# Optimization experiments

Hardware: AMD Instinct MI355X
Metric: run time of the kernel (lower is better)

The kernel has to match this reference:

```python
import jax, jax.numpy as jnp
import numpy as np

B, T, C = 4, 2048, 1024
N_HEAD = 16
HEAD_DIM = C // N_HEAD
SCALE = 1.0 / np.sqrt(HEAD_DIM).astype(np.float32)


def setup_inputs() -> dict:
    key = jax.random.key(0)
    k1, k2, k3 = jax.random.split(key, 3)
    x = jax.random.normal(k1, (B, T, C), dtype=jnp.float32)
    # torch Linear weights: [out_features, in_features], scaled init
    w_qkv = jax.random.normal(k2, (3 * C, C), dtype=jnp.float32) * (1.0 / np.sqrt(C))
    w_out = jax.random.normal(k3, (C, C), dtype=jnp.float32) * (1.0 / np.sqrt(C))
    b_out = jnp.zeros((C,), dtype=jnp.float32)
    return {"x": x, "w_qkv": w_qkv, "w_out": w_out, "b_out": b_out}


def reference(x, w_qkv, w_out, b_out):
    Bsz, Tlen, Cdim = x.shape
    qkv = jnp.einsum('btc,oc->bto', x, w_qkv)  # [B,T,3C]
    q, k, v = jnp.split(qkv, 3, axis=-1)
    # [B,H,T,D]
    def heads(t):
        return t.reshape(Bsz, Tlen, N_HEAD, HEAD_DIM).transpose(0, 2, 1, 3)
    q, k, v = heads(q), heads(k), heads(v)
    att = jnp.einsum('bhqd,bhkd->bhqk', q, k) * SCALE  # [B,H,T,T]
    causal = jnp.tril(jnp.ones((Tlen, Tlen), dtype=bool))
    att = jnp.where(causal[None, None], att, -jnp.inf)
    att = jax.nn.softmax(att, axis=-1)
    out = jnp.einsum('bhqk,bhkd->bhqd', att, v)
    out = out.transpose(0, 2, 1, 3).reshape(Bsz, Tlen, Cdim)
    out = jnp.einsum('btc,oc->bto', out, w_out) + b_out
    return out
```

## Files before the change

kernel.cpp:

```cpp
#include <hip/hip_runtime.h>
#include <stdint.h>


typedef __attribute__((ext_vector_type(8))) short bf16x8;
typedef __attribute__((ext_vector_type(4))) float f32x4;

#define EXP2F(x) __builtin_amdgcn_exp2f(x)
#define SL2E 0.18033688011112042f
#define FIXED_M 15.0f

template <bool B> struct BoolC { static constexpr bool value = B; };

__device__ __forceinline__ short f2bf(float f) {
  union { float f; unsigned u; } c; c.f = f;
  unsigned u = c.u;
  unsigned r = (u + 0x7fffu + ((u >> 16) & 1u)) >> 16;
  return (short)(unsigned short)r;
}

__device__ __forceinline__ void softmax_pack(const f32x4* sc, bf16x8& pa0, bf16x8& pa1) {
  union U { int i[4]; bf16x8 v; };
  U u0, u1;
#pragma unroll
  for (int j = 0; j < 4; ++j) {
    float p0 = EXP2F(sc[j][0]);
    float p1 = EXP2F(sc[j][1]);
    float p2 = EXP2F(sc[j][2]);
    float p3 = EXP2F(sc[j][3]);
    int w0, w1;
    asm("v_cvt_pk_bf16_f32 %0, %1, %2" : "=v"(w0) : "v"(p0), "v"(p1));
    asm("v_cvt_pk_bf16_f32 %0, %1, %2" : "=v"(w1) : "v"(p2), "v"(p3));
    if (j < 2) { u0.i[j * 2] = w0; u0.i[j * 2 + 1] = w1; }
    else       { u1.i[(j - 2) * 2] = w0; u1.i[(j - 2) * 2 + 1] = w1; }
  }
  pa0 = u0.v;
  pa1 = u1.v;
}

__device__ __forceinline__ void llds16(const short* g, short* l) {
  __builtin_amdgcn_global_load_lds(
      (const __attribute__((address_space(1))) unsigned int*)g,
      (__attribute__((address_space(3))) unsigned int*)l, 16, 0, 0);
}

__global__ __launch_bounds__(256) void cast_all(
    const float* __restrict__ x, const float* __restrict__ wq,
    const float* __restrict__ wo, short* __restrict__ xb,
    short* __restrict__ wqb, short* __restrict__ wob) {
  const int b = blockIdx.x;
  const float* src;
  short* dst;
  int idx;
  if (b < 8192)        { src = x;  dst = xb;  idx = b * 256 + threadIdx.x; }
  else if (b < 11264)  { src = wq; dst = wqb; idx = (b - 8192) * 256 + threadIdx.x; }
  else                 { src = wo; dst = wob; idx = (b - 11264) * 256 + threadIdx.x; }
  float4 f = ((const float4*)src)[idx];
  short4 o;
  o.x = f2bf(f.x); o.y = f2bf(f.y); o.z = f2bf(f.z); o.w = f2bf(f.w);
  ((short4*)dst)[idx] = o;
}

__global__ __launch_bounds__(512) void gemm_qkv(
    const short* __restrict__ A, const short* __restrict__ Bw,
    short* __restrict__ Qo, short* __restrict__ Ko, short* __restrict__ Vt) {
  const int K = 1024;
  __shared__ short smem[49152];
  const int tid = threadIdx.x;
  const int lane = tid & 63;
  const int wave = tid >> 6;
  const int wr = wave >> 1;
  const int wc = wave & 1;
  const int m0 = blockIdx.y * 256;
  const int n0 = blockIdx.x * 128;
  const int mrow = lane & 15;
  const int kq = lane >> 4;

  f32x4 acc[4][4];
#pragma unroll
  for (int i = 0; i < 4; ++i)
#pragma unroll
    for (int j = 0; j < 4; ++j) acc[i][j] = (f32x4){0.f, 0.f, 0.f, 0.f};

  auto stageA = [&](int t, int buf, int ca) {
    const int c = ca * 512 + tid;
    const int row = c >> 3;
    const int sc = (c & 7) ^ (row & 7);
    llds16(A + (size_t)(m0 + row) * K + t * 64 + sc * 8,
           &smem[buf * 24576 + c * 8]);
  };
  auto stageB = [&](int t, int buf, int cb) {
    const int c = cb * 512 + tid;
    const int row = c >> 3;
    const int sc = (c & 7) ^ (row & 7);
    llds16(Bw + (size_t)(n0 + row) * K + t * 64 + sc * 8,
           &smem[buf * 24576 + 16384 + c * 8]);
  };

  auto rdA = [&](const short* lA, int i, int kk) -> bf16x8 {
    const int row = wr * 64 + i * 16 + mrow;
    const int ch = (kq + 4 * kk) ^ (row & 7);
    return *(const bf16x8*)&lA[row * 64 + ch * 8];
  };
  auto rdB = [&](const short* lB, int j, int kk) -> bf16x8 {
    const int row = wc * 64 + j * 16 + mrow;
    const int ch = (kq + 4 * kk) ^ (row & 7);
    return *(const bf16x8*)&lB[row * 64 + ch * 8];
  };

  stageA(0, 0, 0); stageA(0, 0, 1); stageA(0, 0, 2); stageA(0, 0, 3);
  stageB(0, 0, 0); stageB(0, 0, 1);
  asm volatile("s_waitcnt vmcnt(0)" ::: "memory");
  __syncthreads();

#define PHASE_TAIL()                                         \
  __builtin_amdgcn_s_barrier();                              \
  asm volatile("s_waitcnt lgkmcnt(0)" ::: "memory");         \
  __builtin_amdgcn_sched_barrier(0);                         \
  __builtin_amdgcn_s_setprio(1);

#define PHASE_END()                                          \
  __builtin_amdgcn_s_setprio(0);                             \
  __builtin_amdgcn_sched_barrier(0);                         \
  __builtin_amdgcn_s_barrier();

  for (int t = 0; t < 16; ++t) {
    const int buf = t & 1;
    const int nb = buf ^ 1;
    const short* lA = &smem[buf * 24576];
    const short* lB = lA + 16384;
    bf16x8 a0, a1, a2, a3, bf0, bf1, bf2, bf3;

    a0 = rdA(lA, 0, 0); a1 = rdA(lA, 1, 0);
    bf0 = rdB(lB, 0, 0); bf1 = rdB(lB, 1, 0);
    bf2 = rdB(lB, 2, 0); bf3 = rdB(lB, 3, 0);
    if (t < 15) { stageA(t + 1, nb, 0); stageA(t + 1, nb, 1); }
    PHASE_TAIL();
    acc[0][0] = __builtin_amdgcn_mfma_f32_16x16x32_bf16(a0, bf0, acc[0][0], 0, 0, 0);
    acc[0][1] = __builtin_amdgcn_mfma_f32_16x16x32_bf16(a0, bf1, acc[0][1], 0, 0, 0);
    acc[0][2] = __builtin_amdgcn_mfma_f32_16x16x32_bf16(a0, bf2, acc[0][2], 0, 0, 0);
    acc[0][3] = __builtin_amdgcn_mfma_f32_16x16x32_bf16(a0, bf3, acc[0][3], 0, 0, 0);
    acc[1][0] = __builtin_amdgcn_mfma_f32_16x16x32_bf16(a1, bf0, acc[1][0], 0, 0, 0);
    acc[1][1] = __builtin_amdgcn_mfma_f32_16x16x32_bf16(a1, bf1, acc[1][1], 0, 0, 0);
    acc[1][2] = __builtin_amdgcn_mfma_f32_16x16x32_bf16(a1, bf2, acc[1][2], 0, 0, 0);
    acc[1][3] = __builtin_amdgcn_mfma_f32_16x16x32_bf16(a1, bf3, acc[1][3], 0, 0, 0);
    PHASE_END();

    a2 = rdA(lA, 2, 0); a3 = rdA(lA, 3, 0);
    if (t < 15) { stageA(t + 1, nb, 2); stageA(t + 1, nb, 3); }
    PHASE_TAIL();
    acc[2][0] = __builtin_amdgcn_mfma_f32_16x16x32_bf16(a2, bf0, acc[2][0], 0, 0, 0);
    acc[2][1] = __builtin_amdgcn_mfma_f32_16x16x32_bf16(a2, bf1, acc[2][1], 0, 0, 0);
    acc[2][2] = __builtin_amdgcn_mfma_f32_16x16x32_bf16(a2, bf2, acc[2][2], 0, 0, 0);
    acc[2][3] = __builtin_amdgcn_mfma_f32_16x16x32_bf16(a2, bf3, acc[2][3], 0, 0, 0);
    acc[3][0] = __builtin_amdgcn_mfma_f32_16x16x32_bf16(a3, bf0, acc[3][0], 0, 0, 0);
    acc[3][1] = __builtin_amdgcn_mfma_f32_16x16x32_bf16(a3, bf1, acc[3][1], 0, 0, 0);
    acc[3][2] = __builtin_amdgcn_mfma_f32_16x16x32_bf16(a3, bf2, acc[3][2], 0, 0, 0);
    acc[3][3] = __builtin_amdgcn_mfma_f32_16x16x32_bf16(a3, bf3, acc[3][3], 0, 0, 0);
    PHASE_END();

    a0 = rdA(lA, 0, 1); a1 = rdA(lA, 1, 1);
    bf0 = rdB(lB, 0, 1); bf1 = rdB(lB, 1, 1);
    bf2 = rdB(lB, 2, 1); bf3 = rdB(lB, 3, 1);
    if (t < 15) { stageB(t + 1, nb, 0); stageB(t + 1, nb, 1); }
    PHASE_TAIL();
    acc[0][0] = __builtin_amdgcn_mfma_f32_16x16x32_bf16(a0, bf0, acc[0][0], 0, 0, 0);
    acc[0][1] = __builtin_amdgcn_mfma_f32_16x16x32_bf16(a0, bf1, acc[0][1], 0, 0, 0);
    acc[0][2] = __builtin_amdgcn_mfma_f32_16x16x32_bf16(a0, bf2, acc[0][2], 0, 0, 0);
    acc[0][3] = __builtin_amdgcn_mfma_f32_16x16x32_bf16(a0, bf3, acc[0][3], 0, 0, 0);
    acc[1][0] = __builtin_amdgcn_mfma_f32_16x16x32_bf16(a1, bf0, acc[1][0], 0, 0, 0);
    acc[1][1] = __builtin_amdgcn_mfma_f32_16x16x32_bf16(a1, bf1, acc[1][1], 0, 0, 0);
    acc[1][2] = __builtin_amdgcn_mfma_f32_16x16x32_bf16(a1, bf2, acc[1][2], 0, 0, 0);
    acc[1][3] = __builtin_amdgcn_mfma_f32_16x16x32_bf16(a1, bf3, acc[1][3], 0, 0, 0);
    PHASE_END();

    a2 = rdA(lA, 2, 1); a3 = rdA(lA, 3, 1);
    PHASE_TAIL();
    acc[2][0] = __builtin_amdgcn_mfma_f32_16x16x32_bf16(a2, bf0, acc[2][0], 0, 0, 0);
    acc[2][1] = __builtin_amdgcn_mfma_f32_16x16x32_bf16(a2, bf1, acc[2][1], 0, 0, 0);
    acc[2][2] = __builtin_amdgcn_mfma_f32_16x16x32_bf16(a2, bf2, acc[2][2], 0, 0, 0);
    acc[2][3] = __builtin_amdgcn_mfma_f32_16x16x32_bf16(a2, bf3, acc[2][3], 0, 0, 0);
    acc[3][0] = __builtin_amdgcn_mfma_f32_16x16x32_bf16(a3, bf0, acc[3][0], 0, 0, 0);
    acc[3][1] = __builtin_amdgcn_mfma_f32_16x16x32_bf16(a3, bf1, acc[3][1], 0, 0, 0);
    acc[3][2] = __builtin_amdgcn_mfma_f32_16x16x32_bf16(a3, bf2, acc[3][2], 0, 0, 0);
    acc[3][3] = __builtin_amdgcn_mfma_f32_16x16x32_bf16(a3, bf3, acc[3][3], 0, 0, 0);
    __builtin_amdgcn_s_setprio(0);
    __builtin_amdgcn_sched_barrier(0);
    if (t < 15) asm volatile("s_waitcnt vmcnt(0)" ::: "memory");
    __builtin_amdgcn_s_barrier();
  }
#undef PHASE_TAIL
#undef PHASE_END

  __syncthreads();

  const int b = m0 >> 11;
  if (n0 < 2048) {
    const float sc_ = ((n0 >> 10) == 1) ? SL2E : 1.0f;
    short* lC = smem;
#pragma unroll
    for (int i = 0; i < 4; ++i) {
      const int rl = wr * 64 + i * 16 + kq * 4;
#pragma unroll
      for (int j = 0; j < 4; ++j) {
        const int col = wc * 64 + j * 16 + mrow;
#pragma unroll
        for (int r = 0; r < 4; ++r)
          lC[(rl + r) * 132 + col] = f2bf(acc[i][j][r] * sc_);
      }
    }
    __syncthreads();
    short* dst = (n0 >> 10) == 0 ? Qo : Ko;
#pragma unroll
    for (int call = 0; call < 8; ++call) {
      const int cc = call * 512 + tid;
      const int row = cc >> 4;
      const int ch = cc & 15;
      const int t = (m0 & 2047) + row;
      const int c = (n0 + ch * 8) & 1023;
      const int h = c >> 6;
      const int d = c & 63;
      bf16x8 val = *(const bf16x8*)&lC[row * 132 + ch * 8];
      *(bf16x8*)(dst + ((size_t)(b * 16 + h) * 2048 + t) * 64 + d) = val;
    }
  } else {
    short* lCt = smem;
#pragma unroll
    for (int i = 0; i < 4; ++i) {
      const int rl = wr * 64 + i * 16 + kq * 4;
#pragma unroll
      for (int j = 0; j < 4; ++j) {
        const int col = wc * 64 + j * 16 + mrow;
#pragma unroll
        for (int r = 0; r < 4; ++r)
          lCt[col * 264 + rl + r] = f2bf(acc[i][j][r]);
      }
    }
    __syncthreads();
#pragma unroll
    for (int call = 0; call < 8; ++call) {
      const int cc = call * 512 + tid;
      const int col = cc >> 5;
      const int tg = cc & 31;
      const int o = n0 + col;
      const int d = o & 63;
      const int h = (o >> 6) & 15;
      const int t = (m0 & 2047) + tg * 8;
      bf16x8 val = *(const bf16x8*)&lCt[col * 264 + tg * 8];
      *(bf16x8*)(Vt + ((size_t)(b * 16 + h) * 64 + d) * 2048 + t) = val;
    }
  }
}

__global__ __launch_bounds__(256) void gemm_out(
    const short* __restrict__ A, const short* __restrict__ Bw,
    const float* __restrict__ bias, float* __restrict__ Out) {
  const int K = 1024;
  __shared__ short smem[16384];
  const int tid = threadIdx.x;
  const int lane = tid & 63;
  const int wave = tid >> 6;
  const int m0 = blockIdx.y * 128;
  const int n0 = blockIdx.x * 128;
  const int wm = (wave >> 1) * 64;
  const int wn = (wave & 1) * 64;
  const int mrow = lane & 15;
  const int kq = lane >> 4;

  f32x4 acc[4][4];
#pragma unroll
  for (int i = 0; i < 4; ++i)
#pragma unroll
    for (int j = 0; j < 4; ++j) acc[i][j] = (f32x4){0.f, 0.f, 0.f, 0.f};

  auto stage = [&](int it, int buf) {
#pragma unroll
    for (int call = 0; call < 2; ++call) {
      const int cb = call * 256 + wave * 64;
      const int c = cb + lane;
      const int row = c >> 2;
      const int scol = (c & 3) ^ ((row ^ (row >> 2)) & 3);
      llds16(A + (size_t)(m0 + row) * K + it * 32 + scol * 8,
             &smem[buf * 8192 + cb * 8]);
      llds16(Bw + (size_t)(n0 + row) * K + it * 32 + scol * 8,
             &smem[buf * 8192 + 4096 + cb * 8]);
    }
  };

  stage(0, 0);
  __syncthreads();

  for (int it = 0; it < 32; ++it) {
    const int buf = it & 1;
    if (it < 31) stage(it + 1, buf ^ 1);
    const short* lA = &smem[buf * 8192];
    const short* lB = &smem[buf * 8192 + 4096];
    bf16x8 af[4], bfr[4];
#pragma unroll
    for (int i = 0; i < 4; ++i) {
      const int row = wm + i * 16 + mrow;
      af[i] = *(const bf16x8*)&lA[row * 32 + (((kq ^ row ^ (row >> 2)) & 3) * 8)];
    }
#pragma unroll
    for (int j = 0; j < 4; ++j) {
      const int row = wn + j * 16 + mrow;
      bfr[j] = *(const bf16x8*)&lB[row * 32 + (((kq ^ row ^ (row >> 2)) & 3) * 8)];
    }
#pragma unroll
    for (int i = 0; i < 4; ++i)
#pragma unroll
      for (int j = 0; j < 4; ++j)
        acc[i][j] = __builtin_amdgcn_mfma_f32_16x16x32_bf16(af[i], bfr[j], acc[i][j], 0, 0, 0);
    __syncthreads();
  }

#pragma unroll
  for (int i = 0; i < 4; ++i) {
    const int m = m0 + wm + i * 16 + kq * 4;
#pragma unroll
    for (int j = 0; j < 4; ++j) {
      const int n = n0 + wn + j * 16 + mrow;
      const float bb = bias[n];
#pragma unroll
      for (int r = 0; r < 4; ++r)
        Out[(size_t)(m + r) * 1024 + n] = acc[i][j][r] + bb;
    }
  }
}

__global__ __launch_bounds__(256) void flash_attn(
    const short* __restrict__ Qg, const short* __restrict__ Kg,
    const short* __restrict__ Vtg, short* __restrict__ Og) {
  const int T = 2048;
  __shared__ short lK[2][64 * 64];
  __shared__ short lVt[2][64 * 64];
  const int tid = threadIdx.x;
  const int lane = tid & 63;
  const int wave = tid >> 6;
  const int bh = blockIdx.x;
  const int bx = blockIdx.y;
  const int mrow = lane & 15;
  const int kq = lane >> 4;
  const int swz = mrow & 7;
  const size_t base = (size_t)bh * T * 64;
  const size_t vbase = (size_t)bh * 64 * T;

  const int qt0 = bx;
  const int qt1 = 31 - bx;

  const bf16x8 ones = {0x3F80, 0x3F80, 0x3F80, 0x3F80, 0x3F80, 0x3F80, 0x3F80, 0x3F80};

  bf16x8 aq0_0, aq1_0, aq0_1, aq1_1;
  {
    const short* qp0 = Qg + base + (size_t)(qt0 * 64 + wave * 16 + mrow) * 64 + kq * 8;
    aq0_0 = *(const bf16x8*)qp0;
    aq1_0 = *(const bf16x8*)(qp0 + 32);
    const short* qp1 = Qg + base + (size_t)(qt1 * 64 + wave * 16 + mrow) * 64 + kq * 8;
    aq0_1 = *(const bf16x8*)qp1;
    aq1_1 = *(const bf16x8*)(qp1 + 32);
  }

  f32x4 acc0[4], acc1[4], lac0, lac1;
  lac0 = (f32x4){0.f, 0.f, 0.f, 0.f};
  lac1 = (f32x4){0.f, 0.f, 0.f, 0.f};
#pragma unroll
  for (int jd = 0; jd < 4; ++jd) {
    acc0[jd] = (f32x4){0.f, 0.f, 0.f, 0.f};
    acc1[jd] = (f32x4){0.f, 0.f, 0.f, 0.f};
  }

  auto stage = [&](int nt, int buf) {
#pragma unroll
    for (int call = 0; call < 2; ++call) {
      const int cb = call * 256 + wave * 64;
      const int c = cb + lane;
      const int row = c >> 3;
      const int scol = (c & 7) ^ (row & 7);
      const int grow = (row & 0x23) | ((row & 0x0C) << 1) | ((row & 0x10) >> 2);
      llds16(Kg + base + (size_t)(nt * 64 + grow) * 64 + scol * 8, &lK[buf][cb * 8]);
      llds16(Vtg + vbase + (size_t)row * T + nt * 64 + scol * 8, &lVt[buf][cb * 8]);
    }
  };

  stage(0, 0);
  __syncthreads();

  auto seg = [&](auto Aa, const short* K_, const short* Vt_, int kt) {
    constexpr bool ACT0 = decltype(Aa)::value;
    f32x4 sc0[4], sc1[4];
#pragma unroll
    for (int j = 0; j < 4; ++j) {
      const short* krow = &K_[(j * 16 + mrow) * 64];
      bf16x8 kb0 = *(const bf16x8*)&krow[(kq ^ swz) * 8];
      bf16x8 kb1 = *(const bf16x8*)&krow[((4 + kq) ^ swz) * 8];
      __builtin_amdgcn_s_setprio(1);
      f32x4 ss = (f32x4){-FIXED_M, -FIXED_M, -FIXED_M, -FIXED_M};
      ss = __builtin_amdgcn_mfma_f32_16x16x32_bf16(kb0, aq0_1, ss, 0, 0, 0);
      ss = __builtin_amdgcn_mfma_f32_16x16x32_bf16(kb1, aq1_1, ss, 0, 0, 0);
      sc1[j] = ss;
      if constexpr (ACT0) {
        f32x4 s2 = (f32x4){-FIXED_M, -FIXED_M, -FIXED_M, -FIXED_M};
        s2 = __builtin_amdgcn_mfma_f32_16x16x32_bf16(kb0, aq0_0, s2, 0, 0, 0);
        s2 = __builtin_amdgcn_mfma_f32_16x16x32_bf16(kb1, aq1_0, s2, 0, 0, 0);
        sc0[j] = s2;
      }
      __builtin_amdgcn_s_setprio(0);
    }

    if (kt == qt1) {
      const int qcol = qt1 * 64 + wave * 16 + mrow;
#pragma unroll
      for (int j = 0; j < 4; ++j) {
        const int keyb = kt * 64 + ((j & 2) << 4) + (kq << 3) + ((j & 1) << 2);
#pragma unroll
        for (int r = 0; r < 4; ++r)
          if (keyb + r > qcol) sc1[j][r] = -1e30f;
      }
    }
    if constexpr (ACT0) {
      if (kt == qt0) {
        const int qcol = qt0 * 64 + wave * 16 + mrow;
#pragma unroll
        for (int j = 0; j < 4; ++j) {
          const int keyb = kt * 64 + ((j & 2) << 4) + (kq << 3) + ((j & 1) << 2);
#pragma unroll
          for (int r = 0; r < 4; ++r)
            if (keyb + r > qcol) sc0[j][r] = -1e30f;
        }
      }
    }

    bf16x8 pa0_1, pa1_1, pa0_0, pa1_0;
    softmax_pack(sc1, pa0_1, pa1_1);
    lac1 = __builtin_amdgcn_mfma_f32_16x16x32_bf16(pa0_1, ones, lac1, 0, 0, 0);
    lac1 = __builtin_amdgcn_mfma_f32_16x16x32_bf16(pa1_1, ones, lac1, 0, 0, 0);
    if constexpr (ACT0) {
      softmax_pack(sc0, pa0_0, pa1_0);
      lac0 = __builtin_amdgcn_mfma_f32_16x16x32_bf16(pa0_0, ones, lac0, 0, 0, 0);
      lac0 = __builtin_amdgcn_mfma_f32_16x16x32_bf16(pa1_0, ones, lac0, 0, 0, 0);
    }

#pragma unroll
    for (int jd = 0; jd < 4; ++jd) {
      const short* vrow = &Vt_[(jd * 16 + mrow) * 64];
      bf16x8 vb0 = *(const bf16x8*)&vrow[(kq ^ swz) * 8];
      bf16x8 vb1 = *(const bf16x8*)&vrow[((4 + kq) ^ swz) * 8];
      __builtin_amdgcn_s_setprio(1);
      acc1[jd] = __builtin_amdgcn_mfma_f32_16x16x32_bf16(pa0_1, vb0, acc1[jd], 0, 0, 0);
      acc1[jd] = __builtin_amdgcn_mfma_f32_16x16x32_bf16(pa1_1, vb1, acc1[jd], 0, 0, 0);
      if constexpr (ACT0) {
        acc0[jd] = __builtin_amdgcn_mfma_f32_16x16x32_bf16(pa0_0, vb0, acc0[jd], 0, 0, 0);
        acc0[jd] = __builtin_amdgcn_mfma_f32_16x16x32_bf16(pa1_0, vb1, acc0[jd], 0, 0, 0);
      }
      __builtin_amdgcn_s_setprio(0);
    }
  };

  for (int kt = 0; kt <= qt1; ++kt) {
    const int bcur = kt & 1;
    if (kt < qt1) stage(kt + 1, bcur ^ 1);
    if (kt <= qt0) seg(BoolC<true>{}, lK[bcur], lVt[bcur], kt);
    else           seg(BoolC<false>{}, lK[bcur], lVt[bcur], kt);
    __syncthreads();
  }

  const int b = bh >> 4;
  const int h = bh & 15;
#pragma unroll
  for (int r = 0; r < 4; ++r) {
    const float inv0 = 1.0f / lac0[r];
    const int t0 = qt0 * 64 + wave * 16 + kq * 4 + r;
#pragma unroll
    for (int jd = 0; jd < 4; ++jd) {
      const int col = h * 64 + jd * 16 + mrow;
      Og[((size_t)b * 2048 + t0) * 1024 + col] = f2bf(acc0[jd][r] * inv0);
    }
    const float inv1 = 1.0f / lac1[r];
    const int t1 = qt1 * 64 + wave * 16 + kq * 4 + r;
#pragma unroll
    for (int jd = 0; jd < 4; ++jd) {
      const int col = h * 64 + jd * 16 + mrow;
      Og[((size_t)b * 2048 + t1) * 1024 + col] = f2bf(acc1[jd][r] * inv1);
    }
  }
}

extern "C" void kernel_launch(void* const* d_in, const int* in_sizes, int n_in,
                              void* d_out, int out_size, void* d_ws, size_t ws_size,
                              hipStream_t stream) {
  const float* x = (const float*)d_in[0];
  const float* w_qkv = (const float*)d_in[1];
  const float* w_out = (const float*)d_in[2];
  const float* b_out = (const float*)d_in[3];
  float* out = (float*)d_out;

  char* ws = (char*)d_ws;
  const size_t NX = 8192ull * 1024;
  const size_t NWQ = 3072ull * 1024;
  const size_t NWO = 1024ull * 1024;
  const size_t NQ = 64ull * 2048 * 64;
  size_t off = 0;
  short* xb    = (short*)(ws + off); off += NX * 2;
  short* wqkvb = (short*)(ws + off); off += NWQ * 2;
  short* woutb = (short*)(ws + off); off += NWO * 2;
  short* q     = (short*)(ws + off); off += NQ * 2;
  short* k     = (short*)(ws + off); off += NQ * 2;
  short* vt    = (short*)(ws + off); off += NQ * 2;
  short* attb  = (short*)(ws + off); off += NX * 2;
  if (off > ws_size) return;

  cast_all<<<12288, 256, 0, stream>>>(x, w_qkv, w_out, xb, wqkvb, woutb);
  gemm_qkv<<<dim3(24, 32), 512, 0, stream>>>(xb, wqkvb, q, k, vt);
  flash_attn<<<dim3(64, 16), 256, 0, stream>>>(q, k, vt, attb);
  gemm_out<<<dim3(8, 64), 256, 0, stream>>>(attb, woutb, b_out, out);
}
```

Before: 248.5 us.

## Process four query tiles per flash-attention block to reuse staged K/V tiles

```diff
diff --git a/kernel.cpp b/kernel.cpp
--- a/kernel.cpp
+++ b/kernel.cpp
@@ -10,6 +10,7 @@
 #define FIXED_M 15.0f
 
 template <bool B> struct BoolC { static constexpr bool value = B; };
+template <int I> struct IntC { static constexpr int value = I; };
 
 __device__ __forceinline__ short f2bf(float f) {
   union { float f; unsigned u; } c; c.f = f;
@@ -344,28 +345,28 @@
   const size_t base = (size_t)bh * T * 64;
   const size_t vbase = (size_t)bh * 64 * T;
 
-  const int qt0 = bx;
-  const int qt1 = 31 - bx;
+  int qts[4];
+  qts[0] = bx;
+  qts[1] = 31 - bx;
+  qts[2] = 15 - bx;
+  qts[3] = 16 + bx;
 
   const bf16x8 ones = {0x3F80, 0x3F80, 0x3F80, 0x3F80, 0x3F80, 0x3F80, 0x3F80, 0x3F80};
 
-  bf16x8 aq0_0, aq1_0, aq0_1, aq1_1;
-  {
-    const short* qp0 = Qg + base + (size_t)(qt0 * 64 + wave * 16 + mrow) * 64 + kq * 8;
-    aq0_0 = *(const bf16x8*)qp0;
-    aq1_0 = *(const bf16x8*)(qp0 + 32);
-    const short* qp1 = Qg + base + (size_t)(qt1 * 64 + wave * 16 + mrow) * 64 + kq * 8;
-    aq0_1 = *(const bf16x8*)qp1;
-    aq1_1 = *(const bf16x8*)(qp1 + 32);
-  }
-
-  f32x4 acc0[4], acc1[4], lac0, lac1;
-  lac0 = (f32x4){0.f, 0.f, 0.f, 0.f};
-  lac1 = (f32x4){0.f, 0.f, 0.f, 0.f};
-#pragma unroll
-  for (int jd = 0; jd < 4; ++jd) {
-    acc0[jd] = (f32x4){0.f, 0.f, 0.f, 0.f};
-    acc1[jd] = (f32x4){0.f, 0.f, 0.f, 0.f};
+  bf16x8 aq0[4], aq1[4];
+#pragma unroll
+  for (int s = 0; s < 4; ++s) {
+    const short* qp = Qg + base + (size_t)(qts[s] * 64 + wave * 16 + mrow) * 64 + kq * 8;
+    aq0[s] = *(const bf16x8*)qp;
+    aq1[s] = *(const bf16x8*)(qp + 32);
+  }
+
+  f32x4 acc[4][4], lac[4];
+#pragma unroll
+  for (int s = 0; s < 4; ++s) {
+    lac[s] = (f32x4){0.f, 0.f, 0.f, 0.f};
+#pragma unroll
+    for (int jd = 0; jd < 4; ++jd) acc[s][jd] = (f32x4){0.f, 0.f, 0.f, 0.f};
   }
 
   auto stage = [&](int nt, int buf) {
@@ -381,11 +382,9 @@
     }
   };
 
-  stage(0, 0);
-  __syncthreads();
-
-  auto seg = [&](auto Aa, const short* K_, const short* Vt_, int kt) {
+  auto seg = [&](auto Aa, auto Pi, const short* K_, const short* Vt_, int kt) {
     constexpr bool ACT0 = decltype(Aa)::value;
+    constexpr int pi = decltype(Pi)::value;
     f32x4 sc0[4], sc1[4];
 #pragma unroll
     for (int j = 0; j < 4; ++j) {
@@ -394,20 +393,20 @@
       bf16x8 kb1 = *(const bf16x8*)&krow[((4 + kq) ^ swz) * 8];
       __builtin_amdgcn_s_setprio(1);
       f32x4 ss = (f32x4){-FIXED_M, -FIXED_M, -FIXED_M, -FIXED_M};
-      ss = __builtin_amdgcn_mfma_f32_16x16x32_bf16(kb0, aq0_1, ss, 0, 0, 0);
-      ss = __builtin_amdgcn_mfma_f32_16x16x32_bf16(kb1, aq1_1, ss, 0, 0, 0);
+      ss = __builtin_amdgcn_mfma_f32_16x16x32_bf16(kb0, aq0[pi + 1], ss, 0, 0, 0);
+      ss = __builtin_amdgcn_mfma_f32_16x16x32_bf16(kb1, aq1[pi + 1], ss, 0, 0, 0);
       sc1[j] = ss;
       if constexpr (ACT0) {
         f32x4 s2 = (f32x4){-FIXED_M, -FIXED_M, -FIXED_M, -FIXED_M};
-        s2 = __builtin_amdgcn_mfma_f32_16x16x32_bf16(kb0, aq0_0, s2, 0, 0, 0);
-        s2 = __builtin_amdgcn_mfma_f32_16x16x32_bf16(kb1, aq1_0, s2, 0, 0, 0);
+        s2 = __builtin_amdgcn_mfma_f32_16x16x32_bf16(kb0, aq0[pi], s2, 0, 0, 0);
+        s2 = __builtin_amdgcn_mfma_f32_16x16x32_bf16(kb1, aq1[pi], s2, 0, 0, 0);
         sc0[j] = s2;
       }
       __builtin_amdgcn_s_setprio(0);
     }
 
-    if (kt == qt1) {
-      const int qcol = qt1 * 64 + wave * 16 + mrow;
+    if (kt == qts[pi + 1]) {
+      const int qcol = qts[pi + 1] * 64 + wave * 16 + mrow;
 #pragma unroll
       for (int j = 0; j < 4; ++j) {
         const int keyb = kt * 64 + ((j & 2) << 4) + (kq << 3) + ((j & 1) << 2);
@@ -417,8 +416,8 @@
       }
     }
     if constexpr (ACT0) {
-      if (kt == qt0) {
-        const int qcol = qt0 * 64 + wave * 16 + mrow;
+      if (kt == qts[pi]) {
+        const int qcol = qts[pi] * 64 + wave * 16 + mrow;
 #pragma unroll
         for (int j = 0; j < 4; ++j) {
           const int keyb = kt * 64 + ((j & 2) << 4) + (kq << 3) + ((j & 1) << 2);
@@ -431,12 +430,12 @@
 
     bf16x8 pa0_1, pa1_1, pa0_0, pa1_0;
     softmax_pack(sc1, pa0_1, pa1_1);
-    lac1 = __builtin_amdgcn_mfma_f32_16x16x32_bf16(pa0_1, ones, lac1, 0, 0, 0);
-    lac1 = __builtin_amdgcn_mfma_f32_16x16x32_bf16(pa1_1, ones, lac1, 0, 0, 0);
+    lac[pi + 1] = __builtin_amdgcn_mfma_f32_16x16x32_bf16(pa0_1, ones, lac[pi + 1], 0, 0, 0);
+    lac[pi + 1] = __builtin_amdgcn_mfma_f32_16x16x32_bf16(pa1_1, ones, lac[pi + 1], 0, 0, 0);
     if constexpr (ACT0) {
       softmax_pack(sc0, pa0_0, pa1_0);
-      lac0 = __builtin_amdgcn_mfma_f32_16x16x32_bf16(pa0_0, ones, lac0, 0, 0, 0);
-      lac0 = __builtin_amdgcn_mfma_f32_16x16x32_bf16(pa1_0, ones, lac0, 0, 0, 0);
+      lac[pi] = __builtin_amdgcn_mfma_f32_16x16x32_bf16(pa0_0, ones, lac[pi], 0, 0, 0);
+      lac[pi] = __builtin_amdgcn_mfma_f32_16x16x32_bf16(pa1_0, ones, lac[pi], 0, 0, 0);
     }
 
 #pragma unroll
@@ -445,41 +444,51 @@
       bf16x8 vb0 = *(const bf16x8*)&vrow[(kq ^ swz) * 8];
       bf16x8 vb1 = *(const bf16x8*)&vrow[((4 + kq) ^ swz) * 8];
       __builtin_amdgcn_s_setprio(1);
-      acc1[jd] = __builtin_amdgcn_mfma_f32_16x16x32_bf16(pa0_1, vb0, acc1[jd], 0, 0, 0);
-      acc1[jd] = __builtin_amdgcn_mfma_f32_16x16x32_bf16(pa1_1, vb1, acc1[jd], 0, 0, 0);
+      acc[pi + 1][jd] = __builtin_amdgcn_mfma_f32_16x16x32_bf16(pa0_1, vb0, acc[pi + 1][jd], 0, 0, 0);
+      acc[pi + 1][jd] = __builtin_amdgcn_mfma_f32_16x16x32_bf16(pa1_1, vb1, acc[pi + 1][jd], 0, 0, 0);
       if constexpr (ACT0) {
-        acc0[jd] = __builtin_amdgcn_mfma_f32_16x16x32_bf16(pa0_0, vb0, acc0[jd], 0, 0, 0);
-        acc0[jd] = __builtin_amdgcn_mfma_f32_16x16x32_bf16(pa1_0, vb1, acc0[jd], 0, 0, 0);
+        acc[pi][jd] = __builtin_amdgcn_mfma_f32_16x16x32_bf16(pa0_0, vb0, acc[pi][jd], 0, 0, 0);
+        acc[pi][jd] = __builtin_amdgcn_mfma_f32_16x16x32_bf16(pa1_0, vb1, acc[pi][jd], 0, 0, 0);
       }
       __builtin_amdgcn_s_setprio(0);
     }
   };
 
-  for (int kt = 0; kt <= qt1; ++kt) {
+  stage(0, 0);
+  const int ktmax = qts[1];
+  for (int kt = 0; kt <= ktmax; ++kt) {
     const int bcur = kt & 1;
-    if (kt < qt1) stage(kt + 1, bcur ^ 1);
-    if (kt <= qt0) seg(BoolC<true>{}, lK[bcur], lVt[bcur], kt);
-    else           seg(BoolC<false>{}, lK[bcur], lVt[bcur], kt);
-    __syncthreads();
+    if (kt < ktmax) {
+      stage(kt + 1, bcur ^ 1);
+      asm volatile("s_waitcnt vmcnt(4)" ::: "memory");
+    } else {
+      asm volatile("s_waitcnt vmcnt(0)" ::: "memory");
+    }
+    __builtin_amdgcn_s_barrier();
+    const short* K_ = lK[bcur];
+    const short* Vt_ = lVt[bcur];
+    if (kt <= qts[0]) seg(BoolC<true>{}, IntC<0>{}, K_, Vt_, kt);
+    else              seg(BoolC<false>{}, IntC<0>{}, K_, Vt_, kt);
+    if (kt <= qts[3]) {
+      if (kt <= qts[2]) seg(BoolC<true>{}, IntC<1 * 2>{}, K_, Vt_, kt);
+      else              seg(BoolC<false>{}, IntC<1 * 2>{}, K_, Vt_, kt);
+    }
+    __builtin_amdgcn_s_barrier();
   }
 
   const int b = bh >> 4;
   const int h = bh & 15;
 #pragma unroll
-  for (int r = 0; r < 4; ++r) {
-    const float inv0 = 1.0f / lac0[r];
-    const int t0 = qt0 * 64 + wave * 16 + kq * 4 + r;
-#pragma unroll
-    for (int jd = 0; jd < 4; ++jd) {
-      const int col = h * 64 + jd * 16 + mrow;
-      Og[((size_t)b * 2048 + t0) * 1024 + col] = f2bf(acc0[jd][r] * inv0);
-    }
-    const float inv1 = 1.0f / lac1[r];
-    const int t1 = qt1 * 64 + wave * 16 + kq * 4 + r;
-#pragma unroll
-    for (int jd = 0; jd < 4; ++jd) {
-      const int col = h * 64 + jd * 16 + mrow;
-      Og[((size_t)b * 2048 + t1) * 1024 + col] = f2bf(acc1[jd][r] * inv1);
+  for (int s = 0; s < 4; ++s) {
+#pragma unroll
+    for (int r = 0; r < 4; ++r) {
+      const float inv = 1.0f / lac[s][r];
+      const int t = qts[s] * 64 + wave * 16 + kq * 4 + r;
+#pragma unroll
+      for (int jd = 0; jd < 4; ++jd) {
+        const int col = h * 64 + jd * 16 + mrow;
+        Og[((size_t)b * 2048 + t) * 1024 + col] = f2bf(acc[s][jd][r] * inv);
+      }
     }
   }
 }
@@ -510,6 +519,6 @@
 
   cast_all<<<12288, 256, 0, stream>>>(x, w_qkv, w_out, xb, wqkvb, woutb);
   gemm_qkv<<<dim3(24, 32), 512, 0, stream>>>(xb, wqkvb, q, k, vt);
-  flash_attn<<<dim3(64, 16), 256, 0, stream>>>(q, k, vt, attb);
+  flash_attn<<<dim3(64, 8), 256, 0, stream>>>(q, k, vt, attb);
   gemm_out<<<dim3(8, 64), 256, 0, stream>>>(attb, woutb, b_out, out);
 }
```

Result: no change. 248.2 us (-0.1%).
